# Optimization experiments

Hardware: AMD Instinct MI355X
Metric: run time of the kernel (lower is better)

## Reference

```python
import jax, jax.numpy as jnp
import numpy as np

NUM_LAYERS = 4  # -> 9 blocks: 4 encoder + bottleneck + 4 decoder
EPS = 1e-6
SQRT2 = float(np.sqrt(2.0))
INV_SQRT3 = float(1.0 / np.sqrt(3.0))


def _block(s, v, W0, W1, Wa, Wb):
    """_SelfInteractionUNet with full_square=False, irreps = Mx0e + Mx1o.

    tensor_square of per-channel (0e+1o):
      0e: s*s ; 0e: |v|^2/sqrt(3) ; 1o: sqrt(2)*s*v ; (2e is produced by e3nn
      but irreps_out has no 2e so the Linear discards it -> omitted here).
    """
    M = s.shape[-1]
    ts0a = s * s                                    # [N, M] 0e
    ts0b = jnp.sum(v * v, axis=-1) * INV_SQRT3      # [N, M] 0e
    ts1 = SQRT2 * s[..., None] * v                  # [N, M, 3] 1o
    s_in = jnp.concatenate([s, ts0a, ts0b], axis=-1)   # [N, 3M]
    v_in = jnp.concatenate([v, ts1], axis=1)           # [N, 2M, 3]
    # irreps-segmented Linear with path (fan-in) normalization
    s2 = (s_in @ W0) * (1.0 / np.sqrt(s_in.shape[-1]))               # [N, Mo]
    v2 = jnp.einsum('ncd,co->nod', v_in, W1) * (1.0 / np.sqrt(v_in.shape[1]))  # [N, Mo, 3]
    Mo = W0.shape[-1]
    # gated MLP on invariants (0e part), silu after each layer
    h = jax.nn.silu((s2 @ Wa) * (1.0 / np.sqrt(Mo)))                 # [N, Mo]
    g = jax.nn.silu((h @ Wb) * (1.0 / np.sqrt(Mo)))                  # [N, 2Mo]
    s2 = s2 * g[:, :Mo]
    v2 = v2 * g[:, Mo:, None]
    return s2, v2


def _eq_layernorm(s, v):
    # scalars: center + RMS normalize; vectors: norm-RMS normalize (equivariant)
    s = s - jnp.mean(s, axis=-1, keepdims=True)
    s = s * jax.lax.rsqrt(jnp.mean(s * s, axis=-1, keepdims=True) + EPS)
    v = v * jax.lax.rsqrt(jnp.mean(v * v, axis=(1, 2), keepdims=True) + EPS)
    return s, v


def _unet(scalars, vectors, W0, W1, Wa, Wb):
    s, v = scalars, vectors
    skips = []
    for i in range(NUM_LAYERS):
        s, v = _block(s, v, W0[i], W1[i], Wa[i], Wb[i])
        s, v = _eq_layernorm(s, v)
        skips.append((s, v))
    s, v = _block(s, v, W0[NUM_LAYERS], W1[NUM_LAYERS], Wa[NUM_LAYERS], Wb[NUM_LAYERS])
    for j in range(NUM_LAYERS):
        ss, vs = skips[NUM_LAYERS - 1 - j]
        s, v = s + ss, v + vs
        k = NUM_LAYERS + 1 + j
        s, v = _block(s, v, W0[k], W1[k], Wa[k], Wb[k])
        if j < NUM_LAYERS - 1:  # no norm on last decoder layer (norm_last=False)
            s, v = _eq_layernorm(s, v)
    N = s.shape[0]
    return jnp.concatenate([s, v.reshape(N, -1)], axis=-1)  # [N, 4M] irreps_array layout


def setup_inputs() -> dict:
    key = jax.random.key(0)
    ks = jax.random.split(key, 6)
    N, M = 16384, 256
    return {
        'scalars': jax.random.normal(ks[0], (N, M), jnp.float32),
        'vectors': jax.random.normal(ks[1], (N, M, 3), jnp.float32),
        'W0': jax.random.normal(ks[2], (9, 3 * M, M), jnp.float32),
        'W1': jax.random.normal(ks[3], (9, 2 * M, M), jnp.float32),
        'Wa': jax.random.normal(ks[4], (9, M, M), jnp.float32),
        'Wb': jax.random.normal(ks[5], (9, M, 2 * M), jnp.float32),
    }


def reference(scalars, vectors, W0, W1, Wa, Wb):
    return _unet(scalars, vectors, W0, W1, Wa, Wb)
```

## Files before the change

kernel.cpp:

```cpp
#include <hip/hip_runtime.h>
#include <hip/hip_bf16.h>
#include <math.h>


typedef __attribute__((ext_vector_type(8))) short bf16x8;
typedef __attribute__((ext_vector_type(4))) short bf16x4;
typedef __attribute__((ext_vector_type(4))) float f32x4;
typedef __attribute__((ext_vector_type(4))) _Float16 f16x4;

__device__ __forceinline__ unsigned asu(float f){ union{float f;unsigned u;}x; x.f=f; return x.u; }
__device__ __forceinline__ float asf(unsigned u){ union{unsigned u;float f;}x; x.u=u; return x.f; }

__device__ __forceinline__ unsigned short f2bf_r(float f){
  unsigned i = asu(f);
  return (unsigned short)((i + 0x7fffu + ((i >> 16) & 1u)) >> 16);
}
__device__ __forceinline__ float bf2f(unsigned short u){ return asf(((unsigned)u) << 16); }

__device__ __forceinline__ void split_t(float f, short& hi, short& lo){
  unsigned u = asu(f);
  hi = (short)(u >> 16);
  float lof = f - asf(u & 0xffff0000u);
  lo = (short)(asu(lof) >> 16);
}
__device__ __forceinline__ float rec(short h, short l){
  return asf(((unsigned)(unsigned short)h) << 16) + asf(((unsigned)(unsigned short)l) << 16);
}
__device__ __forceinline__ f32x4 rec4(const unsigned short* H, const unsigned short* L, size_t o){
  bf16x4 hv = *(const bf16x4*)(H + o);
  bf16x4 lv = *(const bf16x4*)(L + o);
  f32x4 f;
  #pragma unroll
  for (int j = 0; j < 4; ++j) f[j] = rec(hv[j], lv[j]);
  return f;
}

__device__ __forceinline__ int LO(int r, int kc){
  return r * 64 + ((((kc >> 3) ^ (r & 7)) << 3) | (kc & 7));
}

__global__ __launch_bounds__(256)
void transpose_w(const float* __restrict__ W, unsigned short* __restrict__ Wh,
                 unsigned short* __restrict__ Wl, int K, int Mo){
  __shared__ float tile[32][33];
  const int bi = blockIdx.z;
  const float* Wb = W + (size_t)bi * K * Mo;
  const size_t wo = (size_t)bi * K * Mo;
  const int k0 = blockIdx.x * 32, o0 = blockIdx.y * 32;
  const int tx = threadIdx.x & 31, ty = threadIdx.x >> 5;
  #pragma unroll
  for (int i = 0; i < 4; ++i){
    int k = ty + i * 8;
    tile[k][tx] = Wb[(size_t)(k0 + k) * Mo + o0 + tx];
  }
  __syncthreads();
  #pragma unroll
  for (int i = 0; i < 4; ++i){
    int o = ty + i * 8;
    float f = tile[tx][o];
    unsigned short h = f2bf_r(f);
    unsigned short l = f2bf_r(f - bf2f(h));
    Wh[wo + (size_t)(o0 + o) * K + k0 + tx] = h;
    Wl[wo + (size_t)(o0 + o) * K + k0 + tx] = l;
  }
}

__global__ __launch_bounds__(256)
void convert_inputs(const float* __restrict__ s, const float* __restrict__ v,
                    unsigned short* __restrict__ stH, unsigned short* __restrict__ stL,
                    int NM){
  int i = blockIdx.x * 256 + threadIdx.x;
  if (i >= NM) return;
  short h, l;
  split_t(s[i], h, l); stH[i] = h; stL[i] = l;
  const float* vp = v + (size_t)i * 3;
  #pragma unroll
  for (int d = 0; d < 3; ++d){
    split_t(vp[d], h, l);
    stH[(size_t)(1 + d) * NM + i] = h;
    stL[(size_t)(1 + d) * NM + i] = l;
  }
}

__global__ __launch_bounds__(512, 4)
void gemm_sv(const unsigned short* __restrict__ StH, const unsigned short* __restrict__ StL,
             const _Float16* __restrict__ skip,
             const unsigned short* __restrict__ W0h, const unsigned short* __restrict__ W0l,
             const unsigned short* __restrict__ W1h, const unsigned short* __restrict__ W1l,
             unsigned short* __restrict__ s2H, unsigned short* __restrict__ s2L,
             unsigned short* __restrict__ v2H, unsigned short* __restrict__ v2L,
             int NM, float cs, float cv)
{
  __shared__ unsigned short Ash[128*64], Asl[128*64], Bsh[128*64], Bsl[128*64];
  const int tid = threadIdx.x;
  const int lane = tid & 63, wave = tid >> 6;
  const int wm = (wave >> 1) * 32, wn = (wave & 1) * 64;
  const int row0 = blockIdx.x * 128;
  const int z = blockIdx.y;
  const bool isS = (z < 2);
  const int dv = (z - 2) >> 1;
  const int col0 = isS ? z * 128 : ((z - 2) & 1) * 128;
  const int K = isS ? 768 : 512;
  const float scale = isS ? cs : cv;
  const unsigned short* Bhg = isS ? W0h : W1h;
  const unsigned short* Blg = isS ? W0l : W1l;
  unsigned short* outH = isS ? s2H : v2H + (size_t)dv * NM;
  unsigned short* outL = isS ? s2L : v2L + (size_t)dv * NM;
  const bool sk = (skip != nullptr);

  f32x4 acc[2][4];
  #pragma unroll
  for (int m = 0; m < 2; ++m){
    #pragma unroll
    for (int n = 0; n < 4; ++n) acc[m][n] = (f32x4){0.f,0.f,0.f,0.f};
  }

  const int bc = tid >> 2, bk = (tid & 3) * 16;
  const int arr = bc, akc = bk;

  for (int k0 = 0; k0 < K; k0 += 64){
    {
      const size_t o = (size_t)(col0 + bc) * K + k0 + bk;
      bf16x8 x0 = *(const bf16x8*)(Bhg + o);
      bf16x8 x1 = *(const bf16x8*)(Bhg + o + 8);
      bf16x8 y0 = *(const bf16x8*)(Blg + o);
      bf16x8 y1 = *(const bf16x8*)(Blg + o + 8);
      *(bf16x8*)(&Bsh[LO(bc, bk)])     = x0;
      *(bf16x8*)(&Bsh[LO(bc, bk + 8)]) = x1;
      *(bf16x8*)(&Bsl[LO(bc, bk)])     = y0;
      *(bf16x8*)(&Bsl[LO(bc, bk + 8)]) = y1;
    }
    {
      const int gr = row0 + arr;
      const int c  = (k0 + akc) & 255;
      const size_t o = (size_t)gr * 256 + c;
      const int seg = k0 >> 8;
      if (!sk && seg == 0){
        const int p = isS ? 0 : 1 + dv;
        const unsigned short* SH = StH + (size_t)p * NM;
        const unsigned short* SL = StL + (size_t)p * NM;
        *(bf16x8*)(&Ash[LO(arr, akc)])     = *(const bf16x8*)(SH + o);
        *(bf16x8*)(&Ash[LO(arr, akc + 8)]) = *(const bf16x8*)(SH + o + 8);
        *(bf16x8*)(&Asl[LO(arr, akc)])     = *(const bf16x8*)(SL + o);
        *(bf16x8*)(&Asl[LO(arr, akc + 8)]) = *(const bf16x8*)(SL + o + 8);
      } else {
        f32x4 f[4];
        if (isS){
          if (seg <= 1){
            #pragma unroll
            for (int q = 0; q < 4; ++q){
              f32x4 x = rec4(StH, StL, o + 4*q);
              if (sk){
                f16x4 y = *(const f16x4*)(skip + o + 4*q);
                #pragma unroll
                for (int j = 0; j < 4; ++j) x[j] += (float)y[j];
              }
              if (seg == 0){
                f[q] = x;
              } else {
                #pragma unroll
                for (int j = 0; j < 4; ++j) f[q][j] = x[j] * x[j];
              }
            }
          } else {
            #pragma unroll
            for (int q = 0; q < 4; ++q){
              f32x4 a0 = rec4(StH, StL, (size_t)NM + o + 4*q);
              f32x4 a1 = rec4(StH, StL, (size_t)2*NM + o + 4*q);
              f32x4 a2 = rec4(StH, StL, (size_t)3*NM + o + 4*q);
              if (sk){
                f16x4 b0 = *(const f16x4*)(skip + (size_t)NM + o + 4*q);
                f16x4 b1 = *(const f16x4*)(skip + (size_t)2*NM + o + 4*q);
                f16x4 b2 = *(const f16x4*)(skip + (size_t)3*NM + o + 4*q);
                #pragma unroll
                for (int j = 0; j < 4; ++j){
                  a0[j] += (float)b0[j]; a1[j] += (float)b1[j]; a2[j] += (float)b2[j];
                }
              }
              #pragma unroll
              for (int j = 0; j < 4; ++j)
                f[q][j] = (a0[j]*a0[j] + a1[j]*a1[j] + a2[j]*a2[j]) * 0.57735026918962576f;
            }
          }
        } else {
          #pragma unroll
          for (int q = 0; q < 4; ++q){
            f32x4 x = rec4(StH, StL, (size_t)(1 + dv)*NM + o + 4*q);
            if (sk){
              f16x4 y = *(const f16x4*)(skip + (size_t)(1 + dv)*NM + o + 4*q);
              #pragma unroll
              for (int j = 0; j < 4; ++j) x[j] += (float)y[j];
            }
            if (seg == 0){
              f[q] = x;
            } else {
              f32x4 s = rec4(StH, StL, o + 4*q);
              if (sk){
                f16x4 y = *(const f16x4*)(skip + o + 4*q);
                #pragma unroll
                for (int j = 0; j < 4; ++j) s[j] += (float)y[j];
              }
              #pragma unroll
              for (int j = 0; j < 4; ++j) f[q][j] = 1.41421356237309505f * s[j] * x[j];
            }
          }
        }
        #pragma unroll
        for (int q = 0; q < 2; ++q){
          bf16x8 hi, lo;
          #pragma unroll
          for (int j = 0; j < 8; ++j){
            short h, l; split_t(f[q*2 + (j >> 2)][j & 3], h, l);
            hi[j] = h; lo[j] = l;
          }
          *(bf16x8*)(&Ash[LO(arr, akc + q*8)]) = hi;
          *(bf16x8*)(&Asl[LO(arr, akc + q*8)]) = lo;
        }
      }
    }
    __syncthreads();

    const int arow = lane & 15;
    const int ksl  = (lane >> 4) * 8;
    #pragma unroll
    for (int ks = 0; ks < 2; ++ks){
      const int kq = ks * 32 + ksl;
      bf16x8 ah[2], al[2], bh[4], bl[4];
      #pragma unroll
      for (int m = 0; m < 2; ++m){
        const int r = wm + m*16 + arow;
        ah[m] = *(const bf16x8*)(&Ash[LO(r, kq)]);
        al[m] = *(const bf16x8*)(&Asl[LO(r, kq)]);
      }
      #pragma unroll
      for (int n = 0; n < 4; ++n){
        const int r = wn + n*16 + arow;
        bh[n] = *(const bf16x8*)(&Bsh[LO(r, kq)]);
        bl[n] = *(const bf16x8*)(&Bsl[LO(r, kq)]);
      }
      #pragma unroll
      for (int m = 0; m < 2; ++m){
        #pragma unroll
        for (int n = 0; n < 4; ++n){
          acc[m][n] = __builtin_amdgcn_mfma_f32_16x16x32_bf16(ah[m], bh[n], acc[m][n], 0, 0, 0);
          acc[m][n] = __builtin_amdgcn_mfma_f32_16x16x32_bf16(al[m], bh[n], acc[m][n], 0, 0, 0);
          acc[m][n] = __builtin_amdgcn_mfma_f32_16x16x32_bf16(ah[m], bl[n], acc[m][n], 0, 0, 0);
        }
      }
    }
    __syncthreads();
  }

  #pragma unroll
  for (int m = 0; m < 2; ++m){
    #pragma unroll
    for (int n = 0; n < 4; ++n){
      const int cg = col0 + wn + n*16 + (lane & 15);
      #pragma unroll
      for (int j = 0; j < 4; ++j){
        const int rg = row0 + wm + m*16 + ((lane >> 4) * 4) + j;
        short h, l; split_t(acc[m][n][j] * scale, h, l);
        outH[(size_t)rg * 256 + cg] = (unsigned short)h;
        outL[(size_t)rg * 256 + cg] = (unsigned short)l;
      }
    }
  }
}

template<int EPI>
__global__ __launch_bounds__(512, 4)
void gemm_hg(const unsigned short* __restrict__ AhG, const unsigned short* __restrict__ AlG,
             const unsigned short* __restrict__ Bh, const unsigned short* __restrict__ Bl,
             int NM, float scale,
             unsigned short* __restrict__ outH, unsigned short* __restrict__ outL,
             const unsigned short* __restrict__ s2H, const unsigned short* __restrict__ s2L,
             const unsigned short* __restrict__ v2H, const unsigned short* __restrict__ v2L,
             unsigned short* __restrict__ stH, unsigned short* __restrict__ stL,
             float* __restrict__ fout)
{
  __shared__ unsigned short Ash[128*64], Asl[128*64], Bsh[128*64], Bsl[128*64];
  const int tid = threadIdx.x;
  const int lane = tid & 63, wave = tid >> 6;
  const int wm = (wave >> 1) * 32, wn = (wave & 1) * 64;
  const int row0 = blockIdx.x * 128;
  const int col0 = blockIdx.y * 128;
  const int K = 256;

  f32x4 acc[2][4];
  #pragma unroll
  for (int m = 0; m < 2; ++m){
    #pragma unroll
    for (int n = 0; n < 4; ++n) acc[m][n] = (f32x4){0.f,0.f,0.f,0.f};
  }

  const int bc = tid >> 2, bk = (tid & 3) * 16;

  for (int k0 = 0; k0 < K; k0 += 64){
    {
      const size_t o = (size_t)(col0 + bc) * K + k0 + bk;
      bf16x8 x0 = *(const bf16x8*)(Bh + o);
      bf16x8 x1 = *(const bf16x8*)(Bh + o + 8);
      bf16x8 y0 = *(const bf16x8*)(Bl + o);
      bf16x8 y1 = *(const bf16x8*)(Bl + o + 8);
      *(bf16x8*)(&Bsh[LO(bc, bk)])     = x0;
      *(bf16x8*)(&Bsh[LO(bc, bk + 8)]) = x1;
      *(bf16x8*)(&Bsl[LO(bc, bk)])     = y0;
      *(bf16x8*)(&Bsl[LO(bc, bk + 8)]) = y1;
    }
    {
      const size_t o = (size_t)(row0 + bc) * 256 + k0 + bk;
      *(bf16x8*)(&Ash[LO(bc, bk)])     = *(const bf16x8*)(AhG + o);
      *(bf16x8*)(&Ash[LO(bc, bk + 8)]) = *(const bf16x8*)(AhG + o + 8);
      *(bf16x8*)(&Asl[LO(bc, bk)])     = *(const bf16x8*)(AlG + o);
      *(bf16x8*)(&Asl[LO(bc, bk + 8)]) = *(const bf16x8*)(AlG + o + 8);
    }
    __syncthreads();

    const int arow = lane & 15;
    const int ksl  = (lane >> 4) * 8;
    #pragma unroll
    for (int ks = 0; ks < 2; ++ks){
      const int kq = ks * 32 + ksl;
      bf16x8 ah[2], al[2], bh[4], bl[4];
      #pragma unroll
      for (int m = 0; m < 2; ++m){
        const int r = wm + m*16 + arow;
        ah[m] = *(const bf16x8*)(&Ash[LO(r, kq)]);
        al[m] = *(const bf16x8*)(&Asl[LO(r, kq)]);
      }
      #pragma unroll
      for (int n = 0; n < 4; ++n){
        const int r = wn + n*16 + arow;
        bh[n] = *(const bf16x8*)(&Bsh[LO(r, kq)]);
        bl[n] = *(const bf16x8*)(&Bsl[LO(r, kq)]);
      }
      #pragma unroll
      for (int m = 0; m < 2; ++m){
        #pragma unroll
        for (int n = 0; n < 4; ++n){
          acc[m][n] = __builtin_amdgcn_mfma_f32_16x16x32_bf16(ah[m], bh[n], acc[m][n], 0, 0, 0);
          acc[m][n] = __builtin_amdgcn_mfma_f32_16x16x32_bf16(al[m], bh[n], acc[m][n], 0, 0, 0);
          acc[m][n] = __builtin_amdgcn_mfma_f32_16x16x32_bf16(ah[m], bl[n], acc[m][n], 0, 0, 0);
        }
      }
    }
    __syncthreads();
  }

  #pragma unroll
  for (int m = 0; m < 2; ++m){
    #pragma unroll
    for (int n = 0; n < 4; ++n){
      const int cg = col0 + wn + n*16 + (lane & 15);
      #pragma unroll
      for (int j = 0; j < 4; ++j){
        const int rg = row0 + wm + m*16 + ((lane >> 4) * 4) + j;
        float val = acc[m][n][j] * scale;
        if (EPI == 1){
          float sl = val / (1.f + expf(-val));
          short h, l; split_t(sl, h, l);
          outH[(size_t)rg * 256 + cg] = (unsigned short)h;
          outL[(size_t)rg * 256 + cg] = (unsigned short)l;
        } else {
          float gv = val / (1.f + expf(-val));
          if (cg < 256){
            const size_t o = (size_t)rg * 256 + cg;
            float sval = rec(s2H[o], s2L[o]) * gv;
            if (EPI == 2){
              short h, l; split_t(sval, h, l);
              stH[o] = (unsigned short)h; stL[o] = (unsigned short)l;
            } else {
              fout[(size_t)rg * 1024 + cg] = sval;
            }
          } else {
            const int c = cg - 256;
            #pragma unroll
            for (int d = 0; d < 3; ++d){
              const size_t o = (size_t)d * NM + (size_t)rg * 256 + c;
              float vv = rec(v2H[o], v2L[o]) * gv;
              if (EPI == 2){
                short h, l; split_t(vv, h, l);
                stH[(size_t)(1+d) * NM + (size_t)rg * 256 + c] = (unsigned short)h;
                stL[(size_t)(1+d) * NM + (size_t)rg * 256 + c] = (unsigned short)l;
              } else {
                fout[(size_t)rg * 1024 + 256 + 3 * (size_t)c + d] = vv;
              }
            }
          }
        }
      }
    }
  }
}

__global__ __launch_bounds__(256)
void ln_k(unsigned short* __restrict__ stH, unsigned short* __restrict__ stL,
          _Float16* __restrict__ snap, int NM){
  const int row  = blockIdx.x * 4 + (threadIdx.x >> 6);
  const int lane = threadIdx.x & 63;
  const size_t o = (size_t)row * 256 + lane * 4;
  f32x4 sv = rec4(stH, stL, o);
  f32x4 v0 = rec4(stH, stL, (size_t)NM + o);
  f32x4 v1 = rec4(stH, stL, (size_t)2*NM + o);
  f32x4 v2 = rec4(stH, stL, (size_t)3*NM + o);
  float r0 = 0.f, r1 = 0.f, r2 = 0.f;
  #pragma unroll
  for (int j = 0; j < 4; ++j){
    r0 += sv[j];
    r1 += sv[j] * sv[j];
    r2 += v0[j]*v0[j] + v1[j]*v1[j] + v2[j]*v2[j];
  }
  #pragma unroll
  for (int off = 1; off < 64; off <<= 1){
    r0 += __shfl_xor(r0, off, 64);
    r1 += __shfl_xor(r1, off, 64);
    r2 += __shfl_xor(r2, off, 64);
  }
  float mu  = r0 * (1.f / 256.f);
  float var = r1 * (1.f / 256.f) - mu * mu;
  float srs = rsqrtf(var + 1e-6f);
  float vrs = rsqrtf(r2 * (1.f / 768.f) + 1e-6f);
  f32x4 pl[4];
  #pragma unroll
  for (int j = 0; j < 4; ++j){
    pl[0][j] = (sv[j] - mu) * srs;
    pl[1][j] = v0[j] * vrs; pl[2][j] = v1[j] * vrs; pl[3][j] = v2[j] * vrs;
  }
  #pragma unroll
  for (int p = 0; p < 4; ++p){
    bf16x4 hv, lv; f16x4 hx;
    #pragma unroll
    for (int j = 0; j < 4; ++j){
      short h, l; split_t(pl[p][j], h, l);
      hv[j] = h; lv[j] = l; hx[j] = (_Float16)pl[p][j];
    }
    *(bf16x4*)(stH + (size_t)p*NM + o) = hv;
    *(bf16x4*)(stL + (size_t)p*NM + o) = lv;
    if (snap) *(f16x4*)(snap + (size_t)p*NM + o) = hx;
  }
}

extern "C" void kernel_launch(void* const* d_in, const int* in_sizes, int n_in,
                              void* d_out, int out_size, void* d_ws, size_t ws_size,
                              hipStream_t stream){
  const float* s_in = (const float*)d_in[0];
  const float* v_in = (const float*)d_in[1];
  const float* W0 = (const float*)d_in[2];
  const float* W1 = (const float*)d_in[3];
  const float* Wa = (const float*)d_in[4];
  const float* Wb = (const float*)d_in[5];
  const int Mdim = 256;
  const int N  = in_sizes[0] / Mdim;
  const int NM = N * Mdim;

  unsigned short* ws = (unsigned short*)d_ws;
  size_t off = 0;
  auto alloc = [&](size_t elems){ unsigned short* p = ws + off; off += elems; return p; };
  unsigned short* W0h = alloc((size_t)9 * 768 * 256);
  unsigned short* W0l = alloc((size_t)9 * 768 * 256);
  unsigned short* W1h = alloc((size_t)9 * 512 * 256);
  unsigned short* W1l = alloc((size_t)9 * 512 * 256);
  unsigned short* Wah = alloc((size_t)9 * 256 * 256);
  unsigned short* Wal = alloc((size_t)9 * 256 * 256);
  unsigned short* Wbh = alloc((size_t)9 * 256 * 512);
  unsigned short* Wbl = alloc((size_t)9 * 256 * 512);
  unsigned short* s2H = alloc(NM);
  unsigned short* s2L = alloc(NM);
  unsigned short* v2H = alloc((size_t)3 * NM);
  unsigned short* v2L = alloc((size_t)3 * NM);
  unsigned short* hH  = alloc(NM);
  unsigned short* hL  = alloc(NM);
  _Float16* skips = (_Float16*)(ws + off);
  (void)ws_size;

  unsigned short* stateH = (unsigned short*)d_out;
  unsigned short* stateL = stateH + (size_t)4 * NM;

  dim3 blk(256);
  dim3 blk5(512);
  transpose_w<<<dim3(768/32, 256/32, 9), blk, 0, stream>>>(W0, W0h, W0l, 768, 256);
  transpose_w<<<dim3(512/32, 256/32, 9), blk, 0, stream>>>(W1, W1h, W1l, 512, 256);
  transpose_w<<<dim3(256/32, 256/32, 9), blk, 0, stream>>>(Wa, Wah, Wal, 256, 256);
  transpose_w<<<dim3(256/32, 512/32, 9), blk, 0, stream>>>(Wb, Wbh, Wbl, 256, 512);
  convert_inputs<<<dim3(NM/256), blk, 0, stream>>>(s_in, v_in, stateH, stateL, NM);

  const float c_s2 = 1.f / sqrtf(768.f);
  const float c_v2 = 1.f / sqrtf(512.f);
  const float c_hg = 1.f / 16.f;
  const int gx = N / 128;

  auto run_block = [&](int i, const _Float16* skip, bool fin){
    const unsigned short* w0h = W0h + (size_t)i * 768 * 256;
    const unsigned short* w0l = W0l + (size_t)i * 768 * 256;
    const unsigned short* w1h = W1h + (size_t)i * 512 * 256;
    const unsigned short* w1l = W1l + (size_t)i * 512 * 256;
    const unsigned short* wah = Wah + (size_t)i * 256 * 256;
    const unsigned short* wal = Wal + (size_t)i * 256 * 256;
    const unsigned short* wbh = Wbh + (size_t)i * 256 * 512;
    const unsigned short* wbl = Wbl + (size_t)i * 256 * 512;
    gemm_sv<<<dim3(gx, 8), blk5, 0, stream>>>(stateH, stateL, skip,
                                              w0h, w0l, w1h, w1l,
                                              s2H, s2L, v2H, v2L, NM, c_s2, c_v2);
    gemm_hg<1><<<dim3(gx, 2), blk5, 0, stream>>>(s2H, s2L, wah, wal, NM, c_hg,
                                                 hH, hL, nullptr, nullptr, nullptr, nullptr,
                                                 nullptr, nullptr, nullptr);
    if (!fin)
      gemm_hg<2><<<dim3(gx, 4), blk5, 0, stream>>>(hH, hL, wbh, wbl, NM, c_hg,
                                                   nullptr, nullptr, s2H, s2L, v2H, v2L,
                                                   stateH, stateL, nullptr);
    else
      gemm_hg<3><<<dim3(gx, 4), blk5, 0, stream>>>(hH, hL, wbh, wbl, NM, c_hg,
                                                   nullptr, nullptr, s2H, s2L, v2H, v2L,
                                                   nullptr, nullptr, (float*)d_out);
  };

  for (int i = 0; i < 4; ++i){
    run_block(i, nullptr, false);
    ln_k<<<dim3(N/4), blk, 0, stream>>>(stateH, stateL, skips + (size_t)i * 4 * NM, NM);
  }
  run_block(4, nullptr, false);
  for (int j = 0; j < 4; ++j){
    run_block(5 + j, skips + (size_t)(3 - j) * 4 * NM, j == 3);
    if (j < 3) ln_k<<<dim3(N/4), blk, 0, stream>>>(stateH, stateL, nullptr, NM);
  }
}
```

Before: 2.043 ms.

## Retile GEMMs to full-width N tiles with smaller M and K tiles

Changes the GEMM tiling. Each block now covers the full 256-wide output (gemm_sv) or a 256-wide column slab (gemm_hg), with fewer rows (64 or 32) and a K step of 32 instead of 64. The A-side prologue work (input reconstruction, squaring, skip adds) is no longer repeated across column tiles, and the smaller shared-memory footprint allows raising the occupancy hint to 8 blocks. In exchange, each block reloads the whole B operand for fewer rows and synchronizes twice as often per K.

```diff
diff --git a/kernel.cpp b/kernel.cpp
--- a/kernel.cpp
+++ b/kernel.cpp
@@ -36,7 +36,7 @@
 }
 
 __device__ __forceinline__ int LO(int r, int kc){
-  return r * 64 + ((((kc >> 3) ^ (r & 7)) << 3) | (kc & 7));
+  return r * 32 + ((((kc >> 3) ^ (r & 3)) << 3) | (kc & 7));
 }
 
 __global__ __launch_bounds__(256)
@@ -82,7 +82,7 @@
   }
 }
 
-__global__ __launch_bounds__(512, 4)
+__global__ __launch_bounds__(512, 8)
 void gemm_sv(const unsigned short* __restrict__ StH, const unsigned short* __restrict__ StL,
              const _Float16* __restrict__ skip,
              const unsigned short* __restrict__ W0h, const unsigned short* __restrict__ W0l,
@@ -91,15 +91,14 @@
              unsigned short* __restrict__ v2H, unsigned short* __restrict__ v2L,
              int NM, float cs, float cv)
 {
-  __shared__ unsigned short Ash[128*64], Asl[128*64], Bsh[128*64], Bsl[128*64];
+  __shared__ unsigned short Ash[64*32], Asl[64*32], Bsh[256*32], Bsl[256*32];
   const int tid = threadIdx.x;
   const int lane = tid & 63, wave = tid >> 6;
-  const int wm = (wave >> 1) * 32, wn = (wave & 1) * 64;
-  const int row0 = blockIdx.x * 128;
+  const int wm = (wave >> 2) * 32, wn = (wave & 3) * 64;
+  const int row0 = blockIdx.x * 64;
   const int z = blockIdx.y;
-  const bool isS = (z < 2);
-  const int dv = (z - 2) >> 1;
-  const int col0 = isS ? z * 128 : ((z - 2) & 1) * 128;
+  const bool isS = (z == 0);
+  const int dv = z - 1;
   const int K = isS ? 768 : 512;
   const float scale = isS ? cs : cv;
   const unsigned short* Bhg = isS ? W0h : W1h;
@@ -115,12 +114,12 @@
     for (int n = 0; n < 4; ++n) acc[m][n] = (f32x4){0.f,0.f,0.f,0.f};
   }
 
-  const int bc = tid >> 2, bk = (tid & 3) * 16;
-  const int arr = bc, akc = bk;
-
-  for (int k0 = 0; k0 < K; k0 += 64){
+  const int bc = tid >> 1, bk = (tid & 1) * 16;
+  const int ar = tid >> 3, ac = (tid & 7) * 4;
+
+  for (int k0 = 0; k0 < K; k0 += 32){
     {
-      const size_t o = (size_t)(col0 + bc) * K + k0 + bk;
+      const size_t o = (size_t)bc * K + k0 + bk;
       bf16x8 x0 = *(const bf16x8*)(Bhg + o);
       bf16x8 x1 = *(const bf16x8*)(Bhg + o + 8);
       bf16x8 y0 = *(const bf16x8*)(Blg + o);
@@ -131,122 +130,99 @@
       *(bf16x8*)(&Bsl[LO(bc, bk + 8)]) = y1;
     }
     {
-      const int gr = row0 + arr;
-      const int c  = (k0 + akc) & 255;
+      const int gr = row0 + ar;
+      const int c  = (k0 + ac) & 255;
       const size_t o = (size_t)gr * 256 + c;
       const int seg = k0 >> 8;
       if (!sk && seg == 0){
         const int p = isS ? 0 : 1 + dv;
-        const unsigned short* SH = StH + (size_t)p * NM;
-        const unsigned short* SL = StL + (size_t)p * NM;
-        *(bf16x8*)(&Ash[LO(arr, akc)])     = *(const bf16x8*)(SH + o);
-        *(bf16x8*)(&Ash[LO(arr, akc + 8)]) = *(const bf16x8*)(SH + o + 8);
-        *(bf16x8*)(&Asl[LO(arr, akc)])     = *(const bf16x8*)(SL + o);
-        *(bf16x8*)(&Asl[LO(arr, akc + 8)]) = *(const bf16x8*)(SL + o + 8);
+        *(bf16x4*)(&Ash[LO(ar, ac)]) = *(const bf16x4*)(StH + (size_t)p * NM + o);
+        *(bf16x4*)(&Asl[LO(ar, ac)]) = *(const bf16x4*)(StL + (size_t)p * NM + o);
       } else {
-        f32x4 f[4];
+        f32x4 f;
         if (isS){
           if (seg <= 1){
-            #pragma unroll
-            for (int q = 0; q < 4; ++q){
-              f32x4 x = rec4(StH, StL, o + 4*q);
-              if (sk){
-                f16x4 y = *(const f16x4*)(skip + o + 4*q);
-                #pragma unroll
-                for (int j = 0; j < 4; ++j) x[j] += (float)y[j];
-              }
-              if (seg == 0){
-                f[q] = x;
-              } else {
-                #pragma unroll
-                for (int j = 0; j < 4; ++j) f[q][j] = x[j] * x[j];
-              }
-            }
-          } else {
-            #pragma unroll
-            for (int q = 0; q < 4; ++q){
-              f32x4 a0 = rec4(StH, StL, (size_t)NM + o + 4*q);
-              f32x4 a1 = rec4(StH, StL, (size_t)2*NM + o + 4*q);
-              f32x4 a2 = rec4(StH, StL, (size_t)3*NM + o + 4*q);
-              if (sk){
-                f16x4 b0 = *(const f16x4*)(skip + (size_t)NM + o + 4*q);
-                f16x4 b1 = *(const f16x4*)(skip + (size_t)2*NM + o + 4*q);
-                f16x4 b2 = *(const f16x4*)(skip + (size_t)3*NM + o + 4*q);
-                #pragma unroll
-                for (int j = 0; j < 4; ++j){
-                  a0[j] += (float)b0[j]; a1[j] += (float)b1[j]; a2[j] += (float)b2[j];
-                }
-              }
-              #pragma unroll
-              for (int j = 0; j < 4; ++j)
-                f[q][j] = (a0[j]*a0[j] + a1[j]*a1[j] + a2[j]*a2[j]) * 0.57735026918962576f;
-            }
-          }
-        } else {
-          #pragma unroll
-          for (int q = 0; q < 4; ++q){
-            f32x4 x = rec4(StH, StL, (size_t)(1 + dv)*NM + o + 4*q);
+            f32x4 x = rec4(StH, StL, o);
             if (sk){
-              f16x4 y = *(const f16x4*)(skip + (size_t)(1 + dv)*NM + o + 4*q);
+              f16x4 y = *(const f16x4*)(skip + o);
               #pragma unroll
               for (int j = 0; j < 4; ++j) x[j] += (float)y[j];
             }
             if (seg == 0){
-              f[q] = x;
+              f = x;
             } else {
-              f32x4 s = rec4(StH, StL, o + 4*q);
-              if (sk){
-                f16x4 y = *(const f16x4*)(skip + o + 4*q);
-                #pragma unroll
-                for (int j = 0; j < 4; ++j) s[j] += (float)y[j];
+              #pragma unroll
+              for (int j = 0; j < 4; ++j) f[j] = x[j] * x[j];
+            }
+          } else {
+            f32x4 a0 = rec4(StH, StL, (size_t)NM + o);
+            f32x4 a1 = rec4(StH, StL, (size_t)2*NM + o);
+            f32x4 a2 = rec4(StH, StL, (size_t)3*NM + o);
+            if (sk){
+              f16x4 b0 = *(const f16x4*)(skip + (size_t)NM + o);
+              f16x4 b1 = *(const f16x4*)(skip + (size_t)2*NM + o);
+              f16x4 b2 = *(const f16x4*)(skip + (size_t)3*NM + o);
+              #pragma unroll
+              for (int j = 0; j < 4; ++j){
+                a0[j] += (float)b0[j]; a1[j] += (float)b1[j]; a2[j] += (float)b2[j];
               }
+            }
+            #pragma unroll
+            for (int j = 0; j < 4; ++j)
+              f[j] = (a0[j]*a0[j] + a1[j]*a1[j] + a2[j]*a2[j]) * 0.57735026918962576f;
+          }
+        } else {
+          f32x4 x = rec4(StH, StL, (size_t)(1 + dv)*NM + o);
+          if (sk){
+            f16x4 y = *(const f16x4*)(skip + (size_t)(1 + dv)*NM + o);
+            #pragma unroll
+            for (int j = 0; j < 4; ++j) x[j] += (float)y[j];
+          }
+          if (seg == 0){
+            f = x;
+          } else {
+            f32x4 s = rec4(StH, StL, o);
+            if (sk){
+              f16x4 y = *(const f16x4*)(skip + o);
               #pragma unroll
-              for (int j = 0; j < 4; ++j) f[q][j] = 1.41421356237309505f * s[j] * x[j];
+              for (int j = 0; j < 4; ++j) s[j] += (float)y[j];
             }
+            #pragma unroll
+            for (int j = 0; j < 4; ++j) f[j] = 1.41421356237309505f * s[j] * x[j];
           }
         }
+        bf16x4 hi, lo;
         #pragma unroll
-        for (int q = 0; q < 2; ++q){
-          bf16x8 hi, lo;
-          #pragma unroll
-          for (int j = 0; j < 8; ++j){
-            short h, l; split_t(f[q*2 + (j >> 2)][j & 3], h, l);
-            hi[j] = h; lo[j] = l;
-          }
-          *(bf16x8*)(&Ash[LO(arr, akc + q*8)]) = hi;
-          *(bf16x8*)(&Asl[LO(arr, akc + q*8)]) = lo;
-        }
+        for (int j = 0; j < 4; ++j){ short h, l; split_t(f[j], h, l); hi[j]=h; lo[j]=l; }
+        *(bf16x4*)(&Ash[LO(ar, ac)]) = hi;
+        *(bf16x4*)(&Asl[LO(ar, ac)]) = lo;
       }
     }
     __syncthreads();
 
     const int arow = lane & 15;
-    const int ksl  = (lane >> 4) * 8;
-    #pragma unroll
-    for (int ks = 0; ks < 2; ++ks){
-      const int kq = ks * 32 + ksl;
-      bf16x8 ah[2], al[2], bh[4], bl[4];
-      #pragma unroll
-      for (int m = 0; m < 2; ++m){
-        const int r = wm + m*16 + arow;
-        ah[m] = *(const bf16x8*)(&Ash[LO(r, kq)]);
-        al[m] = *(const bf16x8*)(&Asl[LO(r, kq)]);
-      }
+    const int kq   = (lane >> 4) * 8;
+    bf16x8 ah[2], al[2], bh[4], bl[4];
+    #pragma unroll
+    for (int m = 0; m < 2; ++m){
+      const int r = wm + m*16 + arow;
+      ah[m] = *(const bf16x8*)(&Ash[LO(r, kq)]);
+      al[m] = *(const bf16x8*)(&Asl[LO(r, kq)]);
+    }
+    #pragma unroll
+    for (int n = 0; n < 4; ++n){
+      const int r = wn + n*16 + arow;
+      bh[n] = *(const bf16x8*)(&Bsh[LO(r, kq)]);
+      bl[n] = *(const bf16x8*)(&Bsl[LO(r, kq)]);
+    }
+    #pragma unroll
+    for (int m = 0; m < 2; ++m){
       #pragma unroll
       for (int n = 0; n < 4; ++n){
-        const int r = wn + n*16 + arow;
-        bh[n] = *(const bf16x8*)(&Bsh[LO(r, kq)]);
-        bl[n] = *(const bf16x8*)(&Bsl[LO(r, kq)]);
+        acc[m][n] = __builtin_amdgcn_mfma_f32_16x16x32_bf16(ah[m], bh[n], acc[m][n], 0, 0, 0);
+        acc[m][n] = __builtin_amdgcn_mfma_f32_16x16x32_bf16(al[m], bh[n], acc[m][n], 0, 0, 0);
+        acc[m][n] = __builtin_amdgcn_mfma_f32_16x16x32_bf16(ah[m], bl[n], acc[m][n], 0, 0, 0);
       }
-      #pragma unroll
-      for (int m = 0; m < 2; ++m){
-        #pragma unroll
-        for (int n = 0; n < 4; ++n){
-          acc[m][n] = __builtin_amdgcn_mfma_f32_16x16x32_bf16(ah[m], bh[n], acc[m][n], 0, 0, 0);
-          acc[m][n] = __builtin_amdgcn_mfma_f32_16x16x32_bf16(al[m], bh[n], acc[m][n], 0, 0, 0);
-          acc[m][n] = __builtin_amdgcn_mfma_f32_16x16x32_bf16(ah[m], bl[n], acc[m][n], 0, 0, 0);
-        }
-      }
     }
     __syncthreads();
   }
@@ -255,7 +231,7 @@
   for (int m = 0; m < 2; ++m){
     #pragma unroll
     for (int n = 0; n < 4; ++n){
-      const int cg = col0 + wn + n*16 + (lane & 15);
+      const int cg = wn + n*16 + (lane & 15);
       #pragma unroll
       for (int j = 0; j < 4; ++j){
         const int rg = row0 + wm + m*16 + ((lane >> 4) * 4) + j;
@@ -268,7 +244,7 @@
 }
 
 template<int EPI>
-__global__ __launch_bounds__(512, 4)
+__global__ __launch_bounds__(512, 8)
 void gemm_hg(const unsigned short* __restrict__ AhG, const unsigned short* __restrict__ AlG,
              const unsigned short* __restrict__ Bh, const unsigned short* __restrict__ Bl,
              int NM, float scale,
@@ -278,12 +254,12 @@
              unsigned short* __restrict__ stH, unsigned short* __restrict__ stL,
              float* __restrict__ fout)
 {
-  __shared__ unsigned short Ash[128*64], Asl[128*64], Bsh[128*64], Bsl[128*64];
+  __shared__ unsigned short Ash[32*32], Asl[32*32], Bsh[256*32], Bsl[256*32];
   const int tid = threadIdx.x;
   const int lane = tid & 63, wave = tid >> 6;
-  const int wm = (wave >> 1) * 32, wn = (wave & 1) * 64;
-  const int row0 = blockIdx.x * 128;
-  const int col0 = blockIdx.y * 128;
+  const int wm = (wave >> 2) * 16, wn = (wave & 3) * 64;
+  const int row0 = blockIdx.x * 32;
+  const int col0 = blockIdx.y * 256;
   const int K = 256;
 
   f32x4 acc[2][4];
@@ -293,9 +269,9 @@
     for (int n = 0; n < 4; ++n) acc[m][n] = (f32x4){0.f,0.f,0.f,0.f};
   }
 
-  const int bc = tid >> 2, bk = (tid & 3) * 16;
-
-  for (int k0 = 0; k0 < K; k0 += 64){
+  const int bc = tid >> 1, bk = (tid & 1) * 16;
+
+  for (int k0 = 0; k0 < K; k0 += 32){
     {
       const size_t o = (size_t)(col0 + bc) * K + k0 + bk;
       bf16x8 x0 = *(const bf16x8*)(Bh + o);
@@ -307,84 +283,72 @@
       *(bf16x8*)(&Bsl[LO(bc, bk)])     = y0;
       *(bf16x8*)(&Bsl[LO(bc, bk + 8)]) = y1;
     }
+    if (tid < 256){
+      const int ar = tid >> 3, ac = (tid & 7) * 4;
+      const size_t o = (size_t)(row0 + ar) * 256 + k0 + ac;
+      *(bf16x4*)(&Ash[LO(ar, ac)]) = *(const bf16x4*)(AhG + o);
+      *(bf16x4*)(&Asl[LO(ar, ac)]) = *(const bf16x4*)(AlG + o);
+    }
+    __syncthreads();
+
+    const int arow = lane & 15;
+    const int kq   = (lane >> 4) * 8;
+    bf16x8 ah, al, bh[4], bl[4];
     {
-      const size_t o = (size_t)(row0 + bc) * 256 + k0 + bk;
-      *(bf16x8*)(&Ash[LO(bc, bk)])     = *(const bf16x8*)(AhG + o);
-      *(bf16x8*)(&Ash[LO(bc, bk + 8)]) = *(const bf16x8*)(AhG + o + 8);
-      *(bf16x8*)(&Asl[LO(bc, bk)])     = *(const bf16x8*)(AlG + o);
-      *(bf16x8*)(&Asl[LO(bc, bk + 8)]) = *(const bf16x8*)(AlG + o + 8);
+      const int r = wm + arow;
+      ah = *(const bf16x8*)(&Ash[LO(r, kq)]);
+      al = *(const bf16x8*)(&Asl[LO(r, kq)]);
+    }
+    #pragma unroll
+    for (int n = 0; n < 4; ++n){
+      const int r = wn + n*16 + arow;
+      bh[n] = *(const bf16x8*)(&Bsh[LO(r, kq)]);
+      bl[n] = *(const bf16x8*)(&Bsl[LO(r, kq)]);
+    }
+    #pragma unroll
+    for (int n = 0; n < 4; ++n){
+      acc[0][n] = __builtin_amdgcn_mfma_f32_16x16x32_bf16(ah, bh[n], acc[0][n], 0, 0, 0);
+      acc[0][n] = __builtin_amdgcn_mfma_f32_16x16x32_bf16(al, bh[n], acc[0][n], 0, 0, 0);
+      acc[0][n] = __builtin_amdgcn_mfma_f32_16x16x32_bf16(ah, bl[n], acc[0][n], 0, 0, 0);
     }
     __syncthreads();
-
-    const int arow = lane & 15;
-    const int ksl  = (lane >> 4) * 8;
-    #pragma unroll
-    for (int ks = 0; ks < 2; ++ks){
-      const int kq = ks * 32 + ksl;
-      bf16x8 ah[2], al[2], bh[4], bl[4];
-      #pragma unroll
-      for (int m = 0; m < 2; ++m){
-        const int r = wm + m*16 + arow;
-        ah[m] = *(const bf16x8*)(&Ash[LO(r, kq)]);
-        al[m] = *(const bf16x8*)(&Asl[LO(r, kq)]);
-      }
-      #pragma unroll
-      for (int n = 0; n < 4; ++n){
-        const int r = wn + n*16 + arow;
-        bh[n] = *(const bf16x8*)(&Bsh[LO(r, kq)]);
-        bl[n] = *(const bf16x8*)(&Bsl[LO(r, kq)]);
-      }
-      #pragma unroll
-      for (int m = 0; m < 2; ++m){
-        #pragma unroll
-        for (int n = 0; n < 4; ++n){
-          acc[m][n] = __builtin_amdgcn_mfma_f32_16x16x32_bf16(ah[m], bh[n], acc[m][n], 0, 0, 0);
-          acc[m][n] = __builtin_amdgcn_mfma_f32_16x16x32_bf16(al[m], bh[n], acc[m][n], 0, 0, 0);
-          acc[m][n] = __builtin_amdgcn_mfma_f32_16x16x32_bf16(ah[m], bl[n], acc[m][n], 0, 0, 0);
-        }
-      }
-    }
-    __syncthreads();
-  }
-
-  #pragma unroll
-  for (int m = 0; m < 2; ++m){
-    #pragma unroll
-    for (int n = 0; n < 4; ++n){
-      const int cg = col0 + wn + n*16 + (lane & 15);
-      #pragma unroll
-      for (int j = 0; j < 4; ++j){
-        const int rg = row0 + wm + m*16 + ((lane >> 4) * 4) + j;
-        float val = acc[m][n][j] * scale;
-        if (EPI == 1){
-          float sl = val / (1.f + expf(-val));
-          short h, l; split_t(sl, h, l);
-          outH[(size_t)rg * 256 + cg] = (unsigned short)h;
-          outL[(size_t)rg * 256 + cg] = (unsigned short)l;
+  }
+
+  #pragma unroll
+  for (int n = 0; n < 4; ++n){
+    const int cg = col0 + wn + n*16 + (lane & 15);
+    #pragma unroll
+    for (int j = 0; j < 4; ++j){
+      const int rg = row0 + wm + ((lane >> 4) * 4) + j;
+      float val = acc[0][n][j] * scale;
+      if (EPI == 1){
+        float sl = val / (1.f + expf(-val));
+        short h, l; split_t(sl, h, l);
+        outH[(size_t)rg * 256 + cg] = (unsigned short)h;
+        outL[(size_t)rg * 256 + cg] = (unsigned short)l;
+      } else {
+        float gv = val / (1.f + expf(-val));
+        if (cg < 256){
+          const size_t o = (size_t)rg * 256 + cg;
+          float sval = rec(s2H[o], s2L[o]) * gv;
+          if (EPI == 2){
+            short h, l; split_t(sval, h, l);
+            stH[o] = (unsigned short)h; stL[o] = (unsigned short)l;
+          } else {
+            fout[(size_t)rg * 1024 + cg] = sval;
+          }
         } else {
-          float gv = val / (1.f + expf(-val));
-          if (cg < 256){
-            const size_t o = (size_t)rg * 256 + cg;
-            float sval = rec(s2H[o], s2L[o]) * gv;
+          const int c = cg - 256;
+          #pragma unroll
+          for (int d = 0; d < 3; ++d){
+            const size_t o = (size_t)d * NM + (size_t)rg * 256 + c;
+            float vv = rec(v2H[o], v2L[o]) * gv;
             if (EPI == 2){
-              short h, l; split_t(sval, h, l);
-              stH[o] = (unsigned short)h; stL[o] = (unsigned short)l;
+              short h, l; split_t(vv, h, l);
+              stH[(size_t)(1+d) * NM + (size_t)rg * 256 + c] = (unsigned short)h;
+              stL[(size_t)(1+d) * NM + (size_t)rg * 256 + c] = (unsigned short)l;
             } else {
-              fout[(size_t)rg * 1024 + cg] = sval;
-            }
-          } else {
-            const int c = cg - 256;
-            #pragma unroll
-            for (int d = 0; d < 3; ++d){
-              const size_t o = (size_t)d * NM + (size_t)rg * 256 + c;
-              float vv = rec(v2H[o], v2L[o]) * gv;
-              if (EPI == 2){
-                short h, l; split_t(vv, h, l);
-                stH[(size_t)(1+d) * NM + (size_t)rg * 256 + c] = (unsigned short)h;
-                stL[(size_t)(1+d) * NM + (size_t)rg * 256 + c] = (unsigned short)l;
-              } else {
-                fout[(size_t)rg * 1024 + 256 + 3 * (size_t)c + d] = vv;
-              }
+              fout[(size_t)rg * 1024 + 256 + 3 * (size_t)c + d] = vv;
             }
           }
         }
@@ -487,7 +451,6 @@
   const float c_s2 = 1.f / sqrtf(768.f);
   const float c_v2 = 1.f / sqrtf(512.f);
   const float c_hg = 1.f / 16.f;
-  const int gx = N / 128;
 
   auto run_block = [&](int i, const _Float16* skip, bool fin){
     const unsigned short* w0h = W0h + (size_t)i * 768 * 256;
@@ -498,20 +461,20 @@
     const unsigned short* wal = Wal + (size_t)i * 256 * 256;
     const unsigned short* wbh = Wbh + (size_t)i * 256 * 512;
     const unsigned short* wbl = Wbl + (size_t)i * 256 * 512;
-    gemm_sv<<<dim3(gx, 8), blk5, 0, stream>>>(stateH, stateL, skip,
-                                              w0h, w0l, w1h, w1l,
-                                              s2H, s2L, v2H, v2L, NM, c_s2, c_v2);
-    gemm_hg<1><<<dim3(gx, 2), blk5, 0, stream>>>(s2H, s2L, wah, wal, NM, c_hg,
-                                                 hH, hL, nullptr, nullptr, nullptr, nullptr,
-                                                 nullptr, nullptr, nullptr);
+    gemm_sv<<<dim3(N/64, 4), blk5, 0, stream>>>(stateH, stateL, skip,
+                                                w0h, w0l, w1h, w1l,
+                                                s2H, s2L, v2H, v2L, NM, c_s2, c_v2);
+    gemm_hg<1><<<dim3(N/32, 1), blk5, 0, stream>>>(s2H, s2L, wah, wal, NM, c_hg,
+                                                   hH, hL, nullptr, nullptr, nullptr, nullptr,
+                                                   nullptr, nullptr, nullptr);
     if (!fin)
-      gemm_hg<2><<<dim3(gx, 4), blk5, 0, stream>>>(hH, hL, wbh, wbl, NM, c_hg,
-                                                   nullptr, nullptr, s2H, s2L, v2H, v2L,
-                                                   stateH, stateL, nullptr);
+      gemm_hg<2><<<dim3(N/32, 2), blk5, 0, stream>>>(hH, hL, wbh, wbl, NM, c_hg,
+                                                     nullptr, nullptr, s2H, s2L, v2H, v2L,
+                                                     stateH, stateL, nullptr);
     else
-      gemm_hg<3><<<dim3(gx, 4), blk5, 0, stream>>>(hH, hL, wbh, wbl, NM, c_hg,
-                                                   nullptr, nullptr, s2H, s2L, v2H, v2L,
-                                                   nullptr, nullptr, (float*)d_out);
+      gemm_hg<3><<<dim3(N/32, 2), blk5, 0, stream>>>(hH, hL, wbh, wbl, NM, c_hg,
+                                                     nullptr, nullptr, s2H, s2L, v2H, v2L,
+                                                     nullptr, nullptr, (float*)d_out);
   };
 
   for (int i = 0; i < 4; ++i){
```

Measured after the change: 2.413 ms. 1.18x slower.
